# Performance work log

Measured on AMD Instinct MI355X. Metric: run time of the kernel, lower is better.

Reference implementation:

```python
import jax, jax.numpy as jnp
import numpy as np

B, S, D = 2, 2048, 1024
H, DK = 16, 64


def setup_inputs() -> dict:
    key = jax.random.key(0)
    ks = jax.random.split(key, 5)
    x = jax.random.normal(ks[0], (B, S, D), dtype=jnp.float32)
    attn_w = jax.random.normal(ks[1], (3 * H * DK, D), dtype=jnp.float32) * (1.0 / np.sqrt(D))
    attn_b = jax.random.normal(ks[2], (3 * H * DK,), dtype=jnp.float32) * 0.02
    proj_w = jax.random.normal(ks[3], (D, H * DK), dtype=jnp.float32) * (1.0 / np.sqrt(H * DK))
    proj_b = jax.random.normal(ks[4], (D,), dtype=jnp.float32) * 0.02
    return {"x": x, "attn_w": attn_w, "attn_b": attn_b, "proj_w": proj_w, "proj_b": proj_b}


def reference(x, attn_w, attn_b, proj_w, proj_b):
    b, s, d = x.shape
    # fused QKV projection (torch Linear: x @ W.T + b)
    qkv = x @ attn_w.T + attn_b  # [b, s, 3*H*DK]
    q, k, v = jnp.split(qkv, 3, axis=2)
    # [b, s, H, DK] -> [b, H, s, DK]
    q = q.reshape(b, s, H, DK).transpose(0, 2, 1, 3)
    k = k.reshape(b, s, H, DK).transpose(0, 2, 1, 3)
    v = v.reshape(b, s, H, DK).transpose(0, 2, 1, 3)
    scale = 1.0 / np.sqrt(DK).astype(np.float32)
    scores = jnp.einsum('bhqd,bhkd->bhqk', q, k) * scale  # [b, H, s, s]
    causal = jnp.tril(jnp.ones((s, s), dtype=bool))
    scores = jnp.where(causal, scores, jnp.finfo(scores.dtype).min)
    attn = jax.nn.softmax(scores, axis=-1)
    out = jnp.einsum('bhqk,bhkd->bhqd', attn, v)  # [b, H, s, DK]
    out = out.transpose(0, 2, 1, 3).reshape(b, s, H * DK)
    return out @ proj_w.T + proj_b
```

## Files before the change

### kernel.cpp

```cpp
#include <hip/hip_runtime.h>
#include <hip/hip_bf16.h>
#include <stdint.h>


typedef __bf16 bf16_t;
typedef __bf16 bf16x8 __attribute__((ext_vector_type(8)));
typedef float f32x4 __attribute__((ext_vector_type(4)));

#define B_SZ 2
#define S_LEN 2048
#define D_MODEL 1024
#define N_HEADS 16
#define D_HEAD 64
#define M_ROWS (B_SZ * S_LEN)
#define QKV_N (3 * N_HEADS * D_HEAD)

#define Q_SCALE 0.1803368801111204f

#define OFF_XB  (0ull)
#define OFF_WB  (8ull  << 20)
#define OFF_PWB (14ull << 20)
#define OFF_Q   (16ull << 20)
#define OFF_K   (24ull << 20)
#define OFF_VT  (32ull << 20)
#define OFF_AO  (40ull << 20)

__device__ __forceinline__ unsigned short f2bf_u(float f) {
  union { float f; unsigned u; } v; v.f = f;
  unsigned r = v.u + 0x7fffu + ((v.u >> 16) & 1u);
  return (unsigned short)(r >> 16);
}
__device__ __forceinline__ bf16_t f2bf(float f) {
  unsigned short u = f2bf_u(f);
  return __builtin_bit_cast(bf16_t, u);
}
__device__ __forceinline__ unsigned cvt_pk_bf16(float lo, float hi) {
  unsigned r;
  asm volatile("v_cvt_pk_bf16_f32 %0, %1, %2" : "=v"(r) : "v"(lo), "v"(hi));
  return r;
}

__global__ void cvt3_f32_bf16(const float* __restrict__ sa, bf16_t* __restrict__ da, int n4a,
                              const float* __restrict__ sb, bf16_t* __restrict__ db, int n4b,
                              const float* __restrict__ sc, bf16_t* __restrict__ dc, int n4c) {
  int i = blockIdx.x * blockDim.x + threadIdx.x;
  const float* s; bf16_t* d; int j = i;
  if (i < n4a) { s = sa; d = da; }
  else if ((j = i - n4a) < n4b) { s = sb; d = db; }
  else if ((j = i - n4a - n4b) < n4c) { s = sc; d = dc; }
  else return;
  float4 f = reinterpret_cast<const float4*>(s)[j];
  ushort4 o;
  o.x = f2bf_u(f.x); o.y = f2bf_u(f.y); o.z = f2bf_u(f.z); o.w = f2bf_u(f.w);
  reinterpret_cast<ushort4*>(d)[j] = o;
}

#define BM 128
#define BN 128
#define BK 64

__device__ __forceinline__ void gload_lds16(const bf16_t* g, bf16_t* l) {
  __builtin_amdgcn_global_load_lds((__attribute__((address_space(1))) void*)g,
                                   (__attribute__((address_space(3))) void*)l,
                                   16, 0, 0);
}

__device__ __forceinline__ bf16x8 lds_frag(const bf16_t* lds, int row, int kchunk) {
  int pos = kchunk ^ (row & 7);
  return *reinterpret_cast<const bf16x8*>(lds + row * BK + pos * 8);
}

template <int EPI>
__global__ __launch_bounds__(256, 3) void gemm_bt(
    const bf16_t* __restrict__ A, const bf16_t* __restrict__ Bt,
    const float* __restrict__ bias,
    float* __restrict__ fout,
    bf16_t* __restrict__ qout, bf16_t* __restrict__ kout,
    bf16_t* __restrict__ vtout,
    int M, int N, int K) {
  __shared__ bf16_t As[BM * BK];
  __shared__ bf16_t Bs[BN * BK];
  const int tid = threadIdx.x;
  const int lane = tid & 63;
  const int wid = tid >> 6;
  const int wr = wid >> 1, wc = wid & 1;
  const int cl = lane & 15, hl = lane >> 4;
  const int m0 = blockIdx.y * BM, n0 = blockIdx.x * BN;

  f32x4 acc[4][4];
  #pragma unroll
  for (int m = 0; m < 4; ++m)
    #pragma unroll
    for (int n = 0; n < 4; ++n)
      acc[m][n] = (f32x4){0.f, 0.f, 0.f, 0.f};

  for (int kt = 0; kt < K; kt += BK) {
    #pragma unroll
    for (int it = 0; it < 4; ++it) {
      int chunk = it * 256 + tid;
      int row = chunk >> 3, cpos = chunk & 7;
      int csrc = cpos ^ (row & 7);
      bf16_t* ldsA = As + (it * 256 + wid * 64) * 8;
      bf16_t* ldsB = Bs + (it * 256 + wid * 64) * 8;
      gload_lds16(A  + (size_t)(m0 + row) * K + kt + csrc * 8, ldsA);
      gload_lds16(Bt + (size_t)(n0 + row) * K + kt + csrc * 8, ldsB);
    }
    __syncthreads();

    bf16x8 af[2][4], bfr[2][4];
    #pragma unroll
    for (int kk = 0; kk < 2; ++kk) {
      #pragma unroll
      for (int m = 0; m < 4; ++m)
        af[kk][m] = lds_frag(As, wr * 64 + m * 16 + cl, kk * 4 + hl);
      #pragma unroll
      for (int n = 0; n < 4; ++n)
        bfr[kk][n] = lds_frag(Bs, wc * 64 + n * 16 + cl, kk * 4 + hl);
    }
    __builtin_amdgcn_s_setprio(1);
    #pragma unroll
    for (int m = 0; m < 4; ++m)
      #pragma unroll
      for (int n = 0; n < 4; ++n) {
        acc[m][n] = __builtin_amdgcn_mfma_f32_16x16x32_bf16(af[0][m], bfr[0][n], acc[m][n], 0, 0, 0);
        acc[m][n] = __builtin_amdgcn_mfma_f32_16x16x32_bf16(af[1][m], bfr[1][n], acc[m][n], 0, 0, 0);
      }
    __builtin_amdgcn_s_setprio(0);
    __syncthreads();
  }

  #pragma unroll
  for (int n = 0; n < 4; ++n) {
    int ng = n0 + wc * 64 + n * 16 + cl;
    float bv = bias[ng];
    if constexpr (EPI == 0) {
      int part = ng >> 10;
      int r = ng & 1023;
      int h = r >> 6, dk = r & 63;
      #pragma unroll
      for (int m = 0; m < 4; ++m)
        #pragma unroll
        for (int j = 0; j < 4; ++j) {
          int mg = m0 + wr * 64 + m * 16 + hl * 4 + j;
          int b = mg >> 11, s = mg & 2047;
          float val = acc[m][n][j] + bv;
          size_t bh = (size_t)(b * N_HEADS + h);
          if (part == 0)
            qout[(bh * S_LEN + s) * D_HEAD + dk] = f2bf(val * Q_SCALE);
          else if (part == 1)
            kout[(bh * S_LEN + s) * D_HEAD + dk] = f2bf(val);
          else
            vtout[(bh * D_HEAD + dk) * S_LEN + s] = f2bf(val);
        }
    } else {
      #pragma unroll
      for (int m = 0; m < 4; ++m)
        #pragma unroll
        for (int j = 0; j < 4; ++j) {
          int mg = m0 + wr * 64 + m * 16 + hl * 4 + j;
          fout[(size_t)mg * N + ng] = acc[m][n][j] + bv;
        }
    }
  }
}

__global__ __launch_bounds__(512, 1) void attn_fwd(
    const bf16_t* __restrict__ q,
    const bf16_t* __restrict__ k,
    const bf16_t* __restrict__ vt,
    bf16_t* __restrict__ ao) {
  const int blk = blockIdx.x;
  const int bh = (blk & 7) * 4 + ((blk >> 3) & 3);
  const int qp = blk >> 5;
  const int tid = threadIdx.x;
  const int lane = tid & 63, w = tid >> 6;
  const int cl = lane & 15, hl = lane >> 4;
  const bf16_t* qb = q + (size_t)bh * S_LEN * D_HEAD;
  const bf16_t* kb = k + (size_t)bh * S_LEN * D_HEAD;
  const bf16_t* vb = vt + (size_t)bh * D_HEAD * S_LEN;
  const int b = bh >> 4, h = bh & 15;

  __shared__ bf16_t kvbuf[2][2][4096];
  __shared__ bf16_t plds[8][16][72];

  const int srow = tid >> 3;
  const int scc = (tid & 7) ^ (srow & 7);
  const int sw = cl & 7;

  #pragma unroll 1
  for (int tile = 0; tile < 2; ++tile) {
    const int qt = tile ? (15 - qp) : qp;
    const int row0 = qt * 128 + w * 16;
    const int ktb = 2 * qt + 1;

    const bf16_t* qr = qb + (size_t)(row0 + cl) * D_HEAD + hl * 8;
    bf16x8 qf0 = *reinterpret_cast<const bf16x8*>(qr);
    bf16x8 qf1 = *reinterpret_cast<const bf16x8*>(qr + 32);

    float mrow = -1e30f, lrow = 0.f;
    f32x4 acco[4];
    #pragma unroll
    for (int db = 0; db < 4; ++db) acco[db] = (f32x4){0.f, 0.f, 0.f, 0.f};

    gload_lds16(kb + (size_t)(0 * 64 + srow) * D_HEAD + scc * 8, &kvbuf[0][0][w << 9]);
    gload_lds16(vb + (size_t)srow * S_LEN + 0 * 64 + scc * 8,    &kvbuf[0][1][w << 9]);
    __syncthreads();

    int cur = 0;
    for (int kt = 0; kt <= ktb; ++kt) {
      if (kt < ktb) {
        gload_lds16(kb + (size_t)((kt + 1) * 64 + srow) * D_HEAD + scc * 8,
                    &kvbuf[cur ^ 1][0][w << 9]);
        gload_lds16(vb + (size_t)srow * S_LEN + (kt + 1) * 64 + scc * 8,
                    &kvbuf[cur ^ 1][1][w << 9]);
      }

      const bool act = (kt * 64) <= (row0 + 15);
      if (act) {
        const bf16_t* kB = kvbuf[cur][0];
        const bf16_t* vB = kvbuf[cur][1];
        bf16x8 kf[4][2], vf[4][2];
        #pragma unroll
        for (int nb = 0; nb < 4; ++nb) {
          const bf16_t* kr = kB + (nb * 16 + cl) * 64;
          kf[nb][0] = *reinterpret_cast<const bf16x8*>(kr + ((hl ^ sw) << 3));
          kf[nb][1] = *reinterpret_cast<const bf16x8*>(kr + (((hl + 4) ^ sw) << 3));
        }
        #pragma unroll
        for (int db = 0; db < 4; ++db) {
          const bf16_t* vr = vB + (db * 16 + cl) * 64;
          vf[db][0] = *reinterpret_cast<const bf16x8*>(vr + ((hl ^ sw) << 3));
          vf[db][1] = *reinterpret_cast<const bf16x8*>(vr + (((hl + 4) ^ sw) << 3));
        }

        f32x4 sacc[4];
        __builtin_amdgcn_s_setprio(1);
        #pragma unroll
        for (int nb = 0; nb < 4; ++nb) {
          f32x4 s = (f32x4){0.f, 0.f, 0.f, 0.f};
          s = __builtin_amdgcn_mfma_f32_16x16x32_bf16(kf[nb][0], qf0, s, 0, 0, 0);
          s = __builtin_amdgcn_mfma_f32_16x16x32_bf16(kf[nb][1], qf1, s, 0, 0, 0);
          sacc[nb] = s;
        }
        __builtin_amdgcn_s_setprio(0);

        const int qrow = row0 + cl;
        if (kt * 64 + 63 > qrow) {
          #pragma unroll
          for (int nb = 0; nb < 4; ++nb)
            #pragma unroll
            for (int jj = 0; jj < 4; ++jj) {
              int kpos = kt * 64 + nb * 16 + hl * 4 + jj;
              if (kpos > qrow) sacc[nb][jj] = -1e30f;
            }
        }
        float tm = sacc[0][0];
        #pragma unroll
        for (int nb = 0; nb < 4; ++nb)
          #pragma unroll
          for (int jj = 0; jj < 4; ++jj)
            tm = fmaxf(tm, sacc[nb][jj]);
        tm = fmaxf(tm, __shfl_xor(tm, 16));
        tm = fmaxf(tm, __shfl_xor(tm, 32));
        if (__any(tm > mrow + 8.f)) {
          float mnew = fmaxf(mrow, tm);
          float corr = __builtin_amdgcn_exp2f(mrow - mnew);
          mrow = mnew;
          lrow *= corr;
          #pragma unroll
          for (int db = 0; db < 4; ++db) acco[db] *= corr;
        }
        float rs = 0.f;
        #pragma unroll
        for (int nb = 0; nb < 4; ++nb)
          #pragma unroll
          for (int jj = 0; jj < 4; ++jj) {
            float p = __builtin_amdgcn_exp2f(sacc[nb][jj] - mrow);
            sacc[nb][jj] = p;
            rs += p;
          }
        rs += __shfl_xor(rs, 16);
        rs += __shfl_xor(rs, 32);
        lrow += rs;
        #pragma unroll
        for (int nb = 0; nb < 4; ++nb) {
          uint2 u;
          u.x = cvt_pk_bf16(sacc[nb][0], sacc[nb][1]);
          u.y = cvt_pk_bf16(sacc[nb][2], sacc[nb][3]);
          *reinterpret_cast<uint2*>(&plds[w][cl][nb * 16 + hl * 4]) = u;
        }

        bf16x8 pf0 = *reinterpret_cast<const bf16x8*>(&plds[w][cl][hl * 8]);
        bf16x8 pf1 = *reinterpret_cast<const bf16x8*>(&plds[w][cl][32 + hl * 8]);
        __builtin_amdgcn_s_setprio(1);
        #pragma unroll
        for (int db = 0; db < 4; ++db) {
          acco[db] = __builtin_amdgcn_mfma_f32_16x16x32_bf16(vf[db][0], pf0, acco[db], 0, 0, 0);
          acco[db] = __builtin_amdgcn_mfma_f32_16x16x32_bf16(vf[db][1], pf1, acco[db], 0, 0, 0);
        }
        __builtin_amdgcn_s_setprio(0);
      }

      __syncthreads();
      cur ^= 1;
    }

    {
      float linv = 1.f / lrow;
      const int qrow = row0 + cl;
      #pragma unroll
      for (int db = 0; db < 4; ++db) {
        uint2 u;
        u.x = cvt_pk_bf16(acco[db][0] * linv, acco[db][1] * linv);
        u.y = cvt_pk_bf16(acco[db][2] * linv, acco[db][3] * linv);
        *reinterpret_cast<uint2*>(
            ao + ((size_t)(b * S_LEN) + qrow) * D_MODEL + h * D_HEAD + db * 16 + hl * 4) = u;
      }
    }
    __syncthreads();
  }
}

extern "C" void kernel_launch(void* const* d_in, const int* in_sizes, int n_in,
                              void* d_out, int out_size, void* d_ws, size_t ws_size,
                              hipStream_t stream) {
  const float* x      = (const float*)d_in[0];
  const float* attn_w = (const float*)d_in[1];
  const float* attn_b = (const float*)d_in[2];
  const float* proj_w = (const float*)d_in[3];
  const float* proj_b = (const float*)d_in[4];
  float* out = (float*)d_out;
  char* ws = (char*)d_ws;

  bf16_t* xb  = (bf16_t*)(ws + OFF_XB);
  bf16_t* wb  = (bf16_t*)(ws + OFF_WB);
  bf16_t* pwb = (bf16_t*)(ws + OFF_PWB);
  bf16_t* qb  = (bf16_t*)(ws + OFF_Q);
  bf16_t* kb  = (bf16_t*)(ws + OFF_K);
  bf16_t* vtb = (bf16_t*)(ws + OFF_VT);
  bf16_t* aob = (bf16_t*)(ws + OFF_AO);

  const int n4a = M_ROWS * D_MODEL / 4;
  const int n4b = QKV_N * D_MODEL / 4;
  const int n4c = D_MODEL * D_MODEL / 4;
  const int n4 = n4a + n4b + n4c;
  cvt3_f32_bf16<<<(n4 + 255) / 256, 256, 0, stream>>>(x, xb, n4a, attn_w, wb, n4b,
                                                      proj_w, pwb, n4c);

  gemm_bt<0><<<dim3(QKV_N / BN, M_ROWS / BM), 256, 0, stream>>>(
      xb, wb, attn_b, nullptr, qb, kb, vtb, M_ROWS, QKV_N, D_MODEL);

  attn_fwd<<<dim3(256), 512, 0, stream>>>(qb, kb, vtb, aob);

  gemm_bt<1><<<dim3(D_MODEL / BN, M_ROWS / BM), 256, 0, stream>>>(
      aob, pwb, proj_b, out, nullptr, nullptr, nullptr, M_ROWS, D_MODEL, D_MODEL);
}
```

Baseline: 118.3 us.

## Double-buffer LDS tiles in GEMM to overlap global loads with MFMA

The bf16 GEMM kernel now keeps two LDS buffers for the A and B tiles. It issues the global-to-LDS loads for the next K tile before computing on the current one, so memory latency can hide behind MFMA work. LDS use doubles to 64KB per block, and launch bounds drop from 3 to 2 blocks per CU, which lowers occupancy. The unused srow/scp variables are leftover clutter.

```diff
diff --git a/kernel.cpp b/kernel.cpp
--- a/kernel.cpp
+++ b/kernel.cpp
@@ -71,15 +71,15 @@
 }
 
 template <int EPI>
-__global__ __launch_bounds__(256, 3) void gemm_bt(
+__global__ __launch_bounds__(256, 2) void gemm_bt(
     const bf16_t* __restrict__ A, const bf16_t* __restrict__ Bt,
     const float* __restrict__ bias,
     float* __restrict__ fout,
     bf16_t* __restrict__ qout, bf16_t* __restrict__ kout,
     bf16_t* __restrict__ vtout,
     int M, int N, int K) {
-  __shared__ bf16_t As[BM * BK];
-  __shared__ bf16_t Bs[BN * BK];
+  __shared__ bf16_t As[2][BM * BK];
+  __shared__ bf16_t Bs[2][BN * BK];
   const int tid = threadIdx.x;
   const int lane = tid & 63;
   const int wid = tid >> 6;
@@ -87,6 +87,9 @@
   const int cl = lane & 15, hl = lane >> 4;
   const int m0 = blockIdx.y * BM, n0 = blockIdx.x * BN;
 
+  const int srow = tid >> 1;
+  const int scp = tid & 1;
+
   f32x4 acc[4][4];
   #pragma unroll
   for (int m = 0; m < 4; ++m)
@@ -94,28 +97,40 @@
     for (int n = 0; n < 4; ++n)
       acc[m][n] = (f32x4){0.f, 0.f, 0.f, 0.f};
 
+  #pragma unroll
+  for (int it = 0; it < 4; ++it) {
+    int chunk = it * 256 + tid;
+    int row = chunk >> 3, cpos = chunk & 7;
+    int csrc = cpos ^ (row & 7);
+    gload_lds16(A  + (size_t)(m0 + row) * K + csrc * 8, As[0] + (it * 256 + wid * 64) * 8);
+    gload_lds16(Bt + (size_t)(n0 + row) * K + csrc * 8, Bs[0] + (it * 256 + wid * 64) * 8);
+  }
+  __syncthreads();
+
+  int cur = 0;
   for (int kt = 0; kt < K; kt += BK) {
-    #pragma unroll
-    for (int it = 0; it < 4; ++it) {
-      int chunk = it * 256 + tid;
-      int row = chunk >> 3, cpos = chunk & 7;
-      int csrc = cpos ^ (row & 7);
-      bf16_t* ldsA = As + (it * 256 + wid * 64) * 8;
-      bf16_t* ldsB = Bs + (it * 256 + wid * 64) * 8;
-      gload_lds16(A  + (size_t)(m0 + row) * K + kt + csrc * 8, ldsA);
-      gload_lds16(Bt + (size_t)(n0 + row) * K + kt + csrc * 8, ldsB);
-    }
-    __syncthreads();
+    if (kt + BK < K) {
+      #pragma unroll
+      for (int it = 0; it < 4; ++it) {
+        int chunk = it * 256 + tid;
+        int row = chunk >> 3, cpos = chunk & 7;
+        int csrc = cpos ^ (row & 7);
+        gload_lds16(A  + (size_t)(m0 + row) * K + kt + BK + csrc * 8,
+                    As[cur ^ 1] + (it * 256 + wid * 64) * 8);
+        gload_lds16(Bt + (size_t)(n0 + row) * K + kt + BK + csrc * 8,
+                    Bs[cur ^ 1] + (it * 256 + wid * 64) * 8);
+      }
+    }
 
     bf16x8 af[2][4], bfr[2][4];
     #pragma unroll
     for (int kk = 0; kk < 2; ++kk) {
       #pragma unroll
       for (int m = 0; m < 4; ++m)
-        af[kk][m] = lds_frag(As, wr * 64 + m * 16 + cl, kk * 4 + hl);
+        af[kk][m] = lds_frag(As[cur], wr * 64 + m * 16 + cl, kk * 4 + hl);
       #pragma unroll
       for (int n = 0; n < 4; ++n)
-        bfr[kk][n] = lds_frag(Bs, wc * 64 + n * 16 + cl, kk * 4 + hl);
+        bfr[kk][n] = lds_frag(Bs[cur], wc * 64 + n * 16 + cl, kk * 4 + hl);
     }
     __builtin_amdgcn_s_setprio(1);
     #pragma unroll
@@ -127,6 +142,7 @@
       }
     __builtin_amdgcn_s_setprio(0);
     __syncthreads();
+    cur ^= 1;
   }
 
   #pragma unroll
```

After: 132.3 us. +11.8%, slower.
